# Performance work log

Measured on AMD Instinct MI355X. Metric: run time of the kernel, lower is better.

Reference implementation:

```python
import jax, jax.numpy as jnp
import numpy as np

WS = 7        # window size
NH = 8        # num heads


def setup_inputs() -> dict:
    key = jax.random.key(0)
    ks = jax.random.split(key, 5)
    B, N, C = 32, 3136, 512
    x = jax.random.normal(ks[0], (B, N, C), dtype=jnp.float32)
    s = 1.0 / np.sqrt(C)
    w_qkv = jax.random.normal(ks[1], (C, 3 * C), dtype=jnp.float32) * s
    b_qkv = jax.random.normal(ks[2], (3 * C,), dtype=jnp.float32) * 0.01
    w_proj = jax.random.normal(ks[3], (C, C), dtype=jnp.float32) * s
    b_proj = jax.random.normal(ks[4], (C,), dtype=jnp.float32) * 0.01
    return {"x": x, "w_qkv": w_qkv, "b_qkv": b_qkv, "w_proj": w_proj, "b_proj": b_proj}


def reference(x, w_qkv, b_qkv, w_proj, b_proj):
    B, N, C = x.shape
    H = W = int(round(N ** 0.5))
    hd = C // NH
    t = WS * WS  # 49 tokens per window
    # window partition: (B,N,C) -> (nW, 49, C)
    xw = x.reshape(B, H // WS, WS, W // WS, WS, C)
    xw = jnp.transpose(xw, (0, 1, 3, 2, 4, 5)).reshape(-1, t, C)
    # qkv projection; NOTE: no head permute (faithful to source), so
    # q,k,v : (nW, 49, NH, hd)
    qkv = (xw @ w_qkv + b_qkv).reshape(-1, t, 3, NH, hd)
    q, k, v = qkv[:, :, 0], qkv[:, :, 1], qkv[:, :, 2]
    # q @ k^T contracts head_dim, attends over heads axis: (nW, 49, NH, NH)
    attn = jnp.einsum('wthd,wtgd->wthg', q, k) * (hd ** -0.5)
    attn = jax.nn.softmax(attn, axis=-1)
    out = jnp.einsum('wthg,wtgd->wthd', attn, v)          # (nW, 49, NH, hd)
    # faithful transpose(1,2).reshape(-1, 49, C) (scrambles layout, as in torch)
    out = jnp.transpose(out, (0, 2, 1, 3)).reshape(-1, t, C)
    out = out @ w_proj + b_proj
    # window merge back to (B, N, C)
    out = out.reshape(B, H // WS, W // WS, WS, WS, C)
    out = jnp.transpose(out, (0, 1, 3, 2, 4, 5)).reshape(B, N, C)
    return out
```

## Files before the change

kernel.cpp:

```cpp
#include <hip/hip_runtime.h>
#include <stdint.h>
#include <stddef.h>

typedef short s16;
typedef __attribute__((ext_vector_type(8))) short short8;
typedef __attribute__((ext_vector_type(4))) float floatx4;

__device__ __forceinline__ float bf2f(short s) {
    union { float f; uint32_t u; } c; c.u = ((uint32_t)(uint16_t)s) << 16; return c.f;
}
__device__ __forceinline__ short f2bf(float f) {
    union { float f; uint32_t u; } c; c.f = f;
    uint32_t u = c.u;
    u += 0x7fffu + ((u >> 16) & 1u);
    return (short)(u >> 16);
}

__global__ __launch_bounds__(256) void cvt_kernel(const float* __restrict__ src,
                                                  s16* __restrict__ dst) {
    size_t i = (size_t)blockIdx.x * 256 + threadIdx.x;
    const floatx4* s4 = (const floatx4*)src;
    floatx4 a = s4[i * 2], b = s4[i * 2 + 1];
    short8 o;
    o[0] = f2bf(a[0]); o[1] = f2bf(a[1]); o[2] = f2bf(a[2]); o[3] = f2bf(a[3]);
    o[4] = f2bf(b[0]); o[5] = f2bf(b[1]); o[6] = f2bf(b[2]); o[7] = f2bf(b[3]);
    ((short8*)dst)[i] = o;
}

__global__ __launch_bounds__(256) void transpose_kernel(const float* __restrict__ w,
                                                        s16* __restrict__ wt,
                                                        int K, int N) {
    int idx = blockIdx.x * 256 + threadIdx.x;
    if (idx >= K * N) return;
    int n = idx / K, k = idx - n * K;
    wt[idx] = f2bf(w[(size_t)k * N + n]);
}

__device__ __forceinline__ const s16* x_row_ptr(const s16* xb, int m) {
    int win = m / 49, t = m - win * 49;
    int b = win >> 6, rem = win & 63, hb = rem >> 3, wb = rem & 7;
    int r = t / 7, c = t - r * 7;
    int n = (hb * 7 + r) * 56 + wb * 7 + c;
    return xb + ((size_t)b * 3136 + n) * 512;
}

template <int MODE>
__global__ __launch_bounds__(512, 2) void gemm_kernel(const s16* __restrict__ A,
                                                      const s16* __restrict__ Bt,
                                                      const float* __restrict__ bias,
                                                      void* __restrict__ outp) {
    constexpr int NT  = (MODE == 0) ? 6 : 2;
    constexpr int CPX = (MODE == 0) ? 294 : 98;

    const int o  = (blockIdx.x & 7) * CPX + (blockIdx.x >> 3);
    const int tm = o / NT, tn = o - tm * NT;

    const int tid = threadIdx.x, wave = tid >> 6, lane = tid & 63;

    __shared__ s16 lA[3][256 * 32];
    __shared__ s16 lB[3][256 * 32];

    const int rloc = wave * 16 + (lane >> 2);
    const int gran = (((lane & 3) ^ ((lane >> 3) & 3)) << 3);
    const s16* a_src[2];
    const s16* b_src[2];
#pragma unroll
    for (int i = 0; i < 2; ++i) {
        int row = i * 128 + rloc;
        if (MODE == 0) a_src[i] = x_row_ptr(A, tm * 256 + row) + gran;
        else           a_src[i] = A + (size_t)(tm * 256 + row) * 512 + gran;
        b_src[i] = Bt + (size_t)(tn * 256 + row) * 512 + gran;
    }

#define STAGE_A(buf, i)                                                         \
    do {                                                                        \
        __builtin_amdgcn_global_load_lds(                                       \
            (const __attribute__((address_space(1))) void*)a_src[i],            \
            (__attribute__((address_space(3))) void*)&lA[buf][(i) * 4096 + wave * 512], \
            16, 0, 0);                                                          \
        a_src[i] += 32;                                                         \
    } while (0)
#define STAGE_B(buf, i)                                                         \
    do {                                                                        \
        __builtin_amdgcn_global_load_lds(                                       \
            (const __attribute__((address_space(1))) void*)b_src[i],            \
            (__attribute__((address_space(3))) void*)&lB[buf][(i) * 4096 + wave * 512], \
            16, 0, 0);                                                          \
        b_src[i] += 32;                                                         \
    } while (0)

    floatx4 acc[8][4];
#pragma unroll
    for (int mt = 0; mt < 8; ++mt)
#pragma unroll
        for (int nt = 0; nt < 4; ++nt)
            acc[mt][nt] = (floatx4){0.f, 0.f, 0.f, 0.f};

    const int wm = wave & 1, wn = wave >> 1;
    const int lm = lane & 15, quad = lane >> 4;
    const int swz = ((quad ^ ((lm >> 1) & 3)) << 3);

    STAGE_A(0, 0); STAGE_A(0, 1); STAGE_B(0, 0); STAGE_B(0, 1);
    STAGE_A(1, 0); STAGE_A(1, 1); STAGE_B(1, 0); STAGE_B(1, 1);
    asm volatile("s_waitcnt vmcnt(4)" ::: "memory");
    __builtin_amdgcn_s_barrier();
    __builtin_amdgcn_sched_barrier(0);

#pragma unroll
    for (int kt = 0; kt < 16; ++kt) {
        const int cur = kt % 3, nxt = (kt + 2) % 3;

        short8 bq[4], af[4];
#pragma unroll
        for (int nt = 0; nt < 4; ++nt)
            bq[nt] = *(const short8*)&lB[cur][(wn * 64 + nt * 16 + lm) * 32 + swz];
#pragma unroll
        for (int mt = 0; mt < 4; ++mt)
            af[mt] = *(const short8*)&lA[cur][(wm * 128 + mt * 16 + lm) * 32 + swz];
        if (kt < 14) { STAGE_A(nxt, 0); STAGE_A(nxt, 1); }

        __builtin_amdgcn_s_barrier();
        asm volatile("s_waitcnt lgkmcnt(0)" ::: "memory");
        __builtin_amdgcn_sched_barrier(0);

        __builtin_amdgcn_s_setprio(1);
#pragma unroll
        for (int mt = 0; mt < 4; ++mt)
#pragma unroll
            for (int nt = 0; nt < 4; ++nt)
                acc[mt][nt] = __builtin_amdgcn_mfma_f32_16x16x32_bf16(
                    af[mt], bq[nt], acc[mt][nt], 0, 0, 0);
        __builtin_amdgcn_s_setprio(0);
        __builtin_amdgcn_s_barrier();
        __builtin_amdgcn_sched_barrier(0);

        short8 ag[4];
#pragma unroll
        for (int mt = 0; mt < 4; ++mt)
            ag[mt] = *(const short8*)&lA[cur][(wm * 128 + (mt + 4) * 16 + lm) * 32 + swz];
        if (kt < 14) { STAGE_B(nxt, 0); STAGE_B(nxt, 1); }

        __builtin_amdgcn_s_barrier();
        asm volatile("s_waitcnt lgkmcnt(0)" ::: "memory");
        __builtin_amdgcn_sched_barrier(0);

        __builtin_amdgcn_s_setprio(1);
#pragma unroll
        for (int mt = 0; mt < 4; ++mt)
#pragma unroll
            for (int nt = 0; nt < 4; ++nt)
                acc[mt + 4][nt] = __builtin_amdgcn_mfma_f32_16x16x32_bf16(
                    ag[mt], bq[nt], acc[mt + 4][nt], 0, 0, 0);
        __builtin_amdgcn_s_setprio(0);

        if (kt < 14)       asm volatile("s_waitcnt vmcnt(4)" ::: "memory");
        else if (kt == 14) asm volatile("s_waitcnt vmcnt(0)" ::: "memory");
        if (kt != 15) {
            __builtin_amdgcn_s_barrier();
            __builtin_amdgcn_sched_barrier(0);
        }
    }
#undef STAGE_A
#undef STAGE_B

    float bv[4];
#pragma unroll
    for (int nt = 0; nt < 4; ++nt)
        bv[nt] = bias[tn * 256 + wn * 64 + nt * 16 + lm];

#pragma unroll
    for (int mt = 0; mt < 8; ++mt) {
        int mbase = tm * 256 + wm * 128 + mt * 16 + quad * 4;
#pragma unroll
        for (int i = 0; i < 4; ++i) {
            int m = mbase + i;
            size_t rowoff;
            if (MODE == 1) {
                int win = m / 49, t = m - win * 49;
                int b = win >> 6, rem = win & 63, hb = rem >> 3, wb = rem & 7;
                int r = t / 7, c = t - r * 7;
                int n = (hb * 7 + r) * 56 + wb * 7 + c;
                rowoff = ((size_t)b * 3136 + n) * 512;
            } else {
                rowoff = (size_t)m * 1536;
            }
#pragma unroll
            for (int nt = 0; nt < 4; ++nt) {
                int coln = tn * 256 + wn * 64 + nt * 16 + lm;
                float v = acc[mt][nt][i] + bv[nt];
                if (MODE == 0) ((s16*)outp)[rowoff + coln] = f2bf(v);
                else           ((float*)outp)[rowoff + coln] = v;
            }
        }
    }
}

__global__ __launch_bounds__(256) void attn_kernel(const s16* __restrict__ qkv,
                                                   s16* __restrict__ attn) {
    const int tid = threadIdx.x, wave = tid >> 6, lane = tid & 63;
    const int m = blockIdx.x * 4 + wave;

    __shared__ s16 sh[4][1536];
    s16* my = sh[wave];
    const s16* row = qkv + (size_t)m * 1536;
#pragma unroll
    for (int i = 0; i < 3; ++i)
        *(short8*)&my[i * 512 + lane * 8] = *(const short8*)&row[i * 512 + lane * 8];
    __syncthreads();

    const int h = lane >> 3, g = lane & 7;
    const s16* qs = my + h * 64;
    const s16* ks = my + 512 + g * 64;
    const s16* vs = my + 1024;

    float s = 0.f;
#pragma unroll
    for (int db = 0; db < 8; ++db) {
        int d0 = ((db + h) & 7) * 8;
        short8 q8 = *(const short8*)&qs[d0];
        short8 k8 = *(const short8*)&ks[d0];
#pragma unroll
        for (int j = 0; j < 8; ++j) s += bf2f(q8[j]) * bf2f(k8[j]);
    }
    s *= 0.125f;

    float mx = s;
    mx = fmaxf(mx, __shfl_xor(mx, 1));
    mx = fmaxf(mx, __shfl_xor(mx, 2));
    mx = fmaxf(mx, __shfl_xor(mx, 4));
    float p = __expf(s - mx);
    float sum = p;
    sum += __shfl_xor(sum, 1);
    sum += __shfl_xor(sum, 2);
    sum += __shfl_xor(sum, 4);
    p /= sum;

    float o[8];
#pragma unroll
    for (int j = 0; j < 8; ++j) o[j] = 0.f;
    const int dgrp = (lane & 7) * 8;
#pragma unroll
    for (int gg = 0; gg < 8; ++gg) {
        float pg = __shfl(p, h * 8 + gg);
        short8 v8 = *(const short8*)&vs[gg * 64 + dgrp];
#pragma unroll
        for (int j = 0; j < 8; ++j) o[j] += pg * bf2f(v8[j]);
    }

    int win = m / 49, t = m - win * 49;
    s16* dst = attn + (size_t)win * 25088 + h * 3136 + t * 64 + dgrp;
    short8 ob;
#pragma unroll
    for (int j = 0; j < 8; ++j) ob[j] = f2bf(o[j]);
    *(short8*)dst = ob;
}

extern "C" void kernel_launch(void* const* d_in, const int* in_sizes, int n_in,
                              void* d_out, int out_size, void* d_ws, size_t ws_size,
                              hipStream_t stream) {
    const float* x      = (const float*)d_in[0];
    const float* w_qkv  = (const float*)d_in[1];
    const float* b_qkv  = (const float*)d_in[2];
    const float* w_proj = (const float*)d_in[3];
    const float* b_proj = (const float*)d_in[4];

    char* ws = (char*)d_ws;
    s16* xbf    = (s16*)ws;
    s16* qkv    = (s16*)(ws + 102760448ull);
    s16* attn   = (s16*)(ws + 102760448ull + 308281344ull);
    s16* wqkvT  = (s16*)(ws + 102760448ull + 308281344ull + 102760448ull);
    s16* wprojT = (s16*)(ws + 102760448ull + 308281344ull + 102760448ull + 1572864ull);

    cvt_kernel<<<25088, 256, 0, stream>>>(x, xbf);
    transpose_kernel<<<3072, 256, 0, stream>>>(w_qkv, wqkvT, 512, 1536);
    transpose_kernel<<<1024, 256, 0, stream>>>(w_proj, wprojT, 512, 512);
    gemm_kernel<0><<<392 * 6, 512, 0, stream>>>(xbf, wqkvT, b_qkv, qkv);
    attn_kernel<<<25088, 256, 0, stream>>>(qkv, attn);
    gemm_kernel<1><<<392 * 2, 512, 0, stream>>>(attn, wprojT, b_proj, d_out);
}
```

Before: 714.1 us.

## Fuse fp32-to-bf16 input conversion into QKV GEMM A-tile loading

Drops the separate conversion kernel and its bf16 copy of x. The QKV GEMM now loads fp32 rows of x into registers, packs them to bf16 with v_cvt_pk_bf16_f32 and writes them into LDS, replacing the direct global-to-LDS loads for A. This removes a full write and re-read of the activation tensor, but the A path now goes through registers, changes the vmcnt accounting and reads twice the bytes per A tile, since x is read six times across N tiles. The weight transpose also becomes a tiled shared-memory transpose for coalesced reads and writes.

```diff
diff --git a/kernel.cpp b/kernel.cpp
--- a/kernel.cpp
+++ b/kernel.cpp
@@ -16,36 +16,45 @@
     return (short)(u >> 16);
 }
 
-__global__ __launch_bounds__(256) void cvt_kernel(const float* __restrict__ src,
-                                                  s16* __restrict__ dst) {
-    size_t i = (size_t)blockIdx.x * 256 + threadIdx.x;
-    const floatx4* s4 = (const floatx4*)src;
-    floatx4 a = s4[i * 2], b = s4[i * 2 + 1];
-    short8 o;
-    o[0] = f2bf(a[0]); o[1] = f2bf(a[1]); o[2] = f2bf(a[2]); o[3] = f2bf(a[3]);
-    o[4] = f2bf(b[0]); o[5] = f2bf(b[1]); o[6] = f2bf(b[2]); o[7] = f2bf(b[3]);
-    ((short8*)dst)[i] = o;
+__device__ __forceinline__ short8 cvt8(floatx4 a, floatx4 b) {
+    union { uint32_t u[4]; short8 s; } r;
+    asm("v_cvt_pk_bf16_f32 %0, %1, %2" : "=v"(r.u[0]) : "v"(a[0]), "v"(a[1]));
+    asm("v_cvt_pk_bf16_f32 %0, %1, %2" : "=v"(r.u[1]) : "v"(a[2]), "v"(a[3]));
+    asm("v_cvt_pk_bf16_f32 %0, %1, %2" : "=v"(r.u[2]) : "v"(b[0]), "v"(b[1]));
+    asm("v_cvt_pk_bf16_f32 %0, %1, %2" : "=v"(r.u[3]) : "v"(b[2]), "v"(b[3]));
+    return r.s;
 }
 
 __global__ __launch_bounds__(256) void transpose_kernel(const float* __restrict__ w,
                                                         s16* __restrict__ wt,
                                                         int K, int N) {
-    int idx = blockIdx.x * 256 + threadIdx.x;
-    if (idx >= K * N) return;
-    int n = idx / K, k = idx - n * K;
-    wt[idx] = f2bf(w[(size_t)k * N + n]);
-}
-
-__device__ __forceinline__ const s16* x_row_ptr(const s16* xb, int m) {
+    __shared__ s16 t[32][33];
+    const int ntile = N >> 5;
+    const int bk = blockIdx.x / ntile, bn = blockIdx.x - bk * ntile;
+    const int r = threadIdx.x >> 5, c = threadIdx.x & 31;
+#pragma unroll
+    for (int i = 0; i < 4; ++i) {
+        int k = bk * 32 + r + i * 8;
+        t[r + i * 8][c] = f2bf(w[(size_t)k * N + bn * 32 + c]);
+    }
+    __syncthreads();
+#pragma unroll
+    for (int i = 0; i < 4; ++i) {
+        int n = bn * 32 + r + i * 8;
+        wt[(size_t)n * K + bk * 32 + c] = t[c][r + i * 8];
+    }
+}
+
+__device__ __forceinline__ size_t x_row_off(int m) {
     int win = m / 49, t = m - win * 49;
     int b = win >> 6, rem = win & 63, hb = rem >> 3, wb = rem & 7;
     int r = t / 7, c = t - r * 7;
     int n = (hb * 7 + r) * 56 + wb * 7 + c;
-    return xb + ((size_t)b * 3136 + n) * 512;
+    return ((size_t)b * 3136 + n) * 512;
 }
 
 template <int MODE>
-__global__ __launch_bounds__(512, 2) void gemm_kernel(const s16* __restrict__ A,
+__global__ __launch_bounds__(512, 2) void gemm_kernel(const void* __restrict__ A,
                                                       const s16* __restrict__ Bt,
                                                       const float* __restrict__ bias,
                                                       void* __restrict__ outp) {
@@ -60,19 +69,31 @@
     __shared__ s16 lA[3][256 * 32];
     __shared__ s16 lB[3][256 * 32];
 
+    const int gran = (((tid & 3) ^ ((tid >> 3) & 3)) << 3);
+
     const int rloc = wave * 16 + (lane >> 2);
-    const int gran = (((lane & 3) ^ ((lane >> 3) & 3)) << 3);
+    const s16* b_src[2];
+#pragma unroll
+    for (int i = 0; i < 2; ++i)
+        b_src[i] = Bt + (size_t)(tn * 256 + i * 128 + rloc) * 512 + gran;
+
+    const float* pa0 = nullptr;
+    const float* pa1 = nullptr;
+    const int arow0 = tid >> 2;
+    if (MODE == 0) {
+        const float* xf = (const float*)A;
+        const int g8 = (tid & 3) * 8;
+        pa0 = xf + x_row_off(tm * 256 + arow0) + g8;
+        pa1 = xf + x_row_off(tm * 256 + arow0 + 128) + g8;
+    }
     const s16* a_src[2];
-    const s16* b_src[2];
-#pragma unroll
-    for (int i = 0; i < 2; ++i) {
-        int row = i * 128 + rloc;
-        if (MODE == 0) a_src[i] = x_row_ptr(A, tm * 256 + row) + gran;
-        else           a_src[i] = A + (size_t)(tm * 256 + row) * 512 + gran;
-        b_src[i] = Bt + (size_t)(tn * 256 + row) * 512 + gran;
-    }
-
-#define STAGE_A(buf, i)                                                         \
+    if (MODE == 1) {
+#pragma unroll
+        for (int i = 0; i < 2; ++i)
+            a_src[i] = (const s16*)A + (size_t)(tm * 256 + i * 128 + rloc) * 512 + gran;
+    }
+
+#define STAGE_A_LDS(buf, i)                                                     \
     do {                                                                        \
         __builtin_amdgcn_global_load_lds(                                       \
             (const __attribute__((address_space(1))) void*)a_src[i],            \
@@ -88,6 +109,17 @@
             16, 0, 0);                                                          \
         b_src[i] += 32;                                                         \
     } while (0)
+#define LOAD_A_F32()                                                            \
+    do {                                                                        \
+        pv0 = *(const floatx4*)pa0; pv1 = *(const floatx4*)(pa0 + 4);           \
+        pv2 = *(const floatx4*)pa1; pv3 = *(const floatx4*)(pa1 + 4);           \
+        pa0 += 32; pa1 += 32;                                                   \
+    } while (0)
+#define WRITE_A_F32(buf)                                                        \
+    do {                                                                        \
+        *(short8*)&lA[buf][arow0 * 32 + gran] = cvt8(pv0, pv1);                 \
+        *(short8*)&lA[buf][(arow0 + 128) * 32 + gran] = cvt8(pv2, pv3);         \
+    } while (0)
 
     floatx4 acc[8][4];
 #pragma unroll
@@ -100,15 +132,28 @@
     const int lm = lane & 15, quad = lane >> 4;
     const int swz = ((quad ^ ((lm >> 1) & 3)) << 3);
 
-    STAGE_A(0, 0); STAGE_A(0, 1); STAGE_B(0, 0); STAGE_B(0, 1);
-    STAGE_A(1, 0); STAGE_A(1, 1); STAGE_B(1, 0); STAGE_B(1, 1);
-    asm volatile("s_waitcnt vmcnt(4)" ::: "memory");
-    __builtin_amdgcn_s_barrier();
-    __builtin_amdgcn_sched_barrier(0);
+    {
+        floatx4 pv0 = {0,0,0,0}, pv1 = {0,0,0,0}, pv2 = {0,0,0,0}, pv3 = {0,0,0,0};
+        if (MODE == 0) {
+            LOAD_A_F32(); WRITE_A_F32(0);
+            STAGE_B(0, 0); STAGE_B(0, 1);
+            LOAD_A_F32(); WRITE_A_F32(1);
+            STAGE_B(1, 0); STAGE_B(1, 1);
+            asm volatile("s_waitcnt vmcnt(2)" ::: "memory");
+        } else {
+            STAGE_A_LDS(0, 0); STAGE_A_LDS(0, 1); STAGE_B(0, 0); STAGE_B(0, 1);
+            STAGE_A_LDS(1, 0); STAGE_A_LDS(1, 1); STAGE_B(1, 0); STAGE_B(1, 1);
+            asm volatile("s_waitcnt vmcnt(4)" ::: "memory");
+        }
+        asm volatile("s_waitcnt lgkmcnt(0)" ::: "memory");
+        __builtin_amdgcn_s_barrier();
+        __builtin_amdgcn_sched_barrier(0);
+    }
 
 #pragma unroll
     for (int kt = 0; kt < 16; ++kt) {
         const int cur = kt % 3, nxt = (kt + 2) % 3;
+        floatx4 pv0 = {0,0,0,0}, pv1 = {0,0,0,0}, pv2 = {0,0,0,0}, pv3 = {0,0,0,0};
 
         short8 bq[4], af[4];
 #pragma unroll
@@ -117,7 +162,10 @@
 #pragma unroll
         for (int mt = 0; mt < 4; ++mt)
             af[mt] = *(const short8*)&lA[cur][(wm * 128 + mt * 16 + lm) * 32 + swz];
-        if (kt < 14) { STAGE_A(nxt, 0); STAGE_A(nxt, 1); }
+        if (kt < 14) {
+            if (MODE == 0) { LOAD_A_F32(); }
+            else           { STAGE_A_LDS(nxt, 0); STAGE_A_LDS(nxt, 1); }
+        }
 
         __builtin_amdgcn_s_barrier();
         asm volatile("s_waitcnt lgkmcnt(0)" ::: "memory");
@@ -138,7 +186,10 @@
 #pragma unroll
         for (int mt = 0; mt < 4; ++mt)
             ag[mt] = *(const short8*)&lA[cur][(wm * 128 + (mt + 4) * 16 + lm) * 32 + swz];
-        if (kt < 14) { STAGE_B(nxt, 0); STAGE_B(nxt, 1); }
+        if (kt < 14) {
+            if (MODE == 0) { WRITE_A_F32(nxt); }
+            STAGE_B(nxt, 0); STAGE_B(nxt, 1);
+        }
 
         __builtin_amdgcn_s_barrier();
         asm volatile("s_waitcnt lgkmcnt(0)" ::: "memory");
@@ -153,15 +204,21 @@
                     ag[mt], bq[nt], acc[mt + 4][nt], 0, 0, 0);
         __builtin_amdgcn_s_setprio(0);
 
-        if (kt < 14)       asm volatile("s_waitcnt vmcnt(4)" ::: "memory");
-        else if (kt == 14) asm volatile("s_waitcnt vmcnt(0)" ::: "memory");
+        if (kt < 14) {
+            if (MODE == 0) asm volatile("s_waitcnt vmcnt(2)" ::: "memory");
+            else           asm volatile("s_waitcnt vmcnt(4)" ::: "memory");
+        } else if (kt == 14) {
+            asm volatile("s_waitcnt vmcnt(0)" ::: "memory");
+        }
         if (kt != 15) {
             __builtin_amdgcn_s_barrier();
             __builtin_amdgcn_sched_barrier(0);
         }
     }
-#undef STAGE_A
+#undef STAGE_A_LDS
 #undef STAGE_B
+#undef LOAD_A_F32
+#undef WRITE_A_F32
 
     float bv[4];
 #pragma unroll
@@ -265,16 +322,14 @@
     const float* b_proj = (const float*)d_in[4];
 
     char* ws = (char*)d_ws;
-    s16* xbf    = (s16*)ws;
-    s16* qkv    = (s16*)(ws + 102760448ull);
-    s16* attn   = (s16*)(ws + 102760448ull + 308281344ull);
-    s16* wqkvT  = (s16*)(ws + 102760448ull + 308281344ull + 102760448ull);
-    s16* wprojT = (s16*)(ws + 102760448ull + 308281344ull + 102760448ull + 1572864ull);
-
-    cvt_kernel<<<25088, 256, 0, stream>>>(x, xbf);
-    transpose_kernel<<<3072, 256, 0, stream>>>(w_qkv, wqkvT, 512, 1536);
-    transpose_kernel<<<1024, 256, 0, stream>>>(w_proj, wprojT, 512, 512);
-    gemm_kernel<0><<<392 * 6, 512, 0, stream>>>(xbf, wqkvT, b_qkv, qkv);
+    s16* qkv    = (s16*)ws;
+    s16* attn   = (s16*)(ws + 308281344ull);
+    s16* wqkvT  = (s16*)(ws + 308281344ull + 102760448ull);
+    s16* wprojT = (s16*)(ws + 308281344ull + 102760448ull + 1572864ull);
+
+    transpose_kernel<<<768, 256, 0, stream>>>(w_qkv, wqkvT, 512, 1536);
+    transpose_kernel<<<256, 256, 0, stream>>>(w_proj, wprojT, 512, 512);
+    gemm_kernel<0><<<392 * 6, 512, 0, stream>>>(x, wqkvT, b_qkv, qkv);
     attn_kernel<<<25088, 256, 0, stream>>>(qkv, attn);
     gemm_kernel<1><<<392 * 2, 512, 0, stream>>>(attn, wprojT, b_proj, d_out);
 }
```

After: 707.8 us. Within noise of the previous version (-0.9%).
